# Optimization experiments

Measured on AMD Instinct MI355X. Metric: run time of the kernel, lower is better.

The kernel has to match this reference:

```python
import jax, jax.numpy as jnp
import numpy as np

B, CIN, H, W = 16, 1024, 32, 32
WIDTH = 256          # bottleneck width = planes * base_width/64 * cardinality
OUT = 1024           # planes * expansion
HEADS = WIDTH // 8   # 32
KS = 3               # kernel_size of SelfAttLayer


def unfold3x3(x):
    # x: (B, C, H, W) -> (B, C, 9, H, W), torch.nn.Unfold(3, padding=1) ordering (row-major kernel)
    xp = jnp.pad(x, ((0, 0), (0, 0), (1, 1), (1, 1)))
    h, w = x.shape[2], x.shape[3]
    patches = [xp[:, :, i:i + h, j:j + w] for i in range(KS) for j in range(KS)]
    return jnp.stack(patches, axis=2)


def bn(x, s, b):
    # inference-mode BatchNorm2d with running stats folded into per-channel scale/bias
    return x * s[None, :, None, None] + b[None, :, None, None]


def conv1x1(x, w):
    # w: (Cout, Cin)
    return jnp.einsum('bchw,oc->bohw', x, w)


def setup_inputs() -> dict:
    key = jax.random.key(0)
    ks = jax.random.split(key, 16)
    f = lambda k, shp, scale: (jax.random.normal(k, shp, dtype=jnp.float32) * scale)
    inp = {
        'x': f(ks[0], (B, CIN, H, W), 1.0),
        'w_conv1': f(ks[1], (WIDTH, CIN), 1.0 / np.sqrt(CIN)),
        'bn1_s': jnp.ones((WIDTH,), jnp.float32), 'bn1_b': jnp.zeros((WIDTH,), jnp.float32),
        'wq': f(ks[2], (WIDTH, WIDTH), 1.0 / np.sqrt(WIDTH)),
        'bnq_s': jnp.ones((WIDTH,), jnp.float32), 'bnq_b': jnp.zeros((WIDTH,), jnp.float32),
        'wk': f(ks[3], (WIDTH, WIDTH), 1.0 / np.sqrt(WIDTH)),
        'bnk_s': jnp.ones((WIDTH,), jnp.float32), 'bnk_b': jnp.zeros((WIDTH,), jnp.float32),
        'wv': f(ks[4], (WIDTH, WIDTH), 1.0 / np.sqrt(WIDTH)),
        'bnv_s': jnp.ones((WIDTH,), jnp.float32), 'bnv_b': jnp.zeros((WIDTH,), jnp.float32),
        'pos_h': f(ks[5], (WIDTH, KS, 1), 1.0),
        'pos_w': f(ks[6], (WIDTH, 1, KS), 1.0),
        'bnatt_s': jnp.ones((WIDTH,), jnp.float32), 'bnatt_b': jnp.zeros((WIDTH,), jnp.float32),
        'w_conv3': f(ks[7], (OUT, WIDTH), 1.0 / np.sqrt(WIDTH)),
        'bn3_s': jnp.ones((OUT,), jnp.float32), 'bn3_b': jnp.zeros((OUT,), jnp.float32),
    }
    return inp


def self_att(x, wq, bnq_s, bnq_b, wk, bnk_s, bnk_b, wv, bnv_s, bnv_b,
             pos_h, pos_w, bnatt_s, bnatt_b):
    b, c, h, w = x.shape
    d = c // HEADS
    q = jax.nn.relu(bn(conv1x1(x, wq), bnq_s, bnq_b))          # (B,C,H,W)
    k = jax.nn.relu(bn(conv1x1(x, wk), bnk_s, bnk_b))          # key_ks=1 -> 1x1 conv
    v = bn(conv1x1(x, wv), bnv_s, bnv_b)
    unfold_k = unfold3x3(k)                                     # (B,C,9,H,W)
    pos = (pos_h + pos_w).reshape(1, c, KS * KS, 1, 1)          # (1,C,9,1,1)
    kp = (unfold_k + pos).reshape(b, HEADS, d, KS * KS, h, w)
    qh = q.reshape(b, HEADS, d, h, w)
    attn = jnp.einsum('bgdhw,bgdkhw->bgkhw', qh, kp)            # (B,heads,9,H,W)
    attn = jax.nn.softmax(attn, axis=2)
    # local conv: each channel-group of size d shares its head's attention weights
    v_unf = unfold3x3(v).reshape(b, HEADS, d, KS * KS, h, w)
    out = jnp.einsum('bgdkhw,bgkhw->bgdhw', v_unf, attn).reshape(b, c, h, w)
    return jax.nn.relu(bn(out, bnatt_s, bnatt_b))


def reference(x, w_conv1, bn1_s, bn1_b, wq, bnq_s, bnq_b, wk, bnk_s, bnk_b,
              wv, bnv_s, bnv_b, pos_h, pos_w, bnatt_s, bnatt_b,
              w_conv3, bn3_s, bn3_b):
    residual = x
    h = jax.nn.relu(bn(conv1x1(x, w_conv1), bn1_s, bn1_b))
    h = self_att(h, wq, bnq_s, bnq_b, wk, bnk_s, bnk_b, wv, bnv_s, bnv_b,
                 pos_h, pos_w, bnatt_s, bnatt_b)
    h = bn(conv1x1(h, w_conv3), bn3_s, bn3_b)
    return jax.nn.relu(h + residual)
```

## Files before the change

kernel.cpp:

```cpp
#include <hip/hip_runtime.h>
#include <stdint.h>


typedef __attribute__((ext_vector_type(4))) float f32x4;
typedef __attribute__((ext_vector_type(8))) __bf16 bf16x8;
typedef __attribute__((ext_vector_type(4))) unsigned short u16x4;
typedef __attribute__((ext_vector_type(8))) unsigned short u16x8;

__device__ __forceinline__ float bf2f(unsigned short u) {
  union { unsigned int i; float f; } c; c.i = ((unsigned int)u) << 16; return c.f;
}
__device__ __forceinline__ unsigned short f2bf(float f) {
  union { float f; unsigned int i; } c; c.f = f;
  unsigned int x = c.i;
  return (unsigned short)((x + 0x7FFFu + ((x >> 16) & 1u)) >> 16);
}

__global__ __launch_bounds__(256) void k_transpose_x(const float* __restrict__ x,
                                                     unsigned short* __restrict__ xt) {
  __shared__ float tile[32][33];
  const int b  = blockIdx.z;
  const int c0 = blockIdx.y * 32;
  const int p0 = blockIdx.x * 32;
  const int tx = threadIdx.x & 31;
  const int ty = threadIdx.x >> 5;
  const float* xb = x + (size_t)b * 1048576;
  unsigned short* xtb = xt + (size_t)b * 1048576;
#pragma unroll
  for (int i = 0; i < 4; ++i)
    tile[ty + i * 8][tx] = xb[(size_t)(c0 + ty + i * 8) * 1024 + p0 + tx];
  __syncthreads();
#pragma unroll
  for (int i = 0; i < 4; ++i)
    xtb[(size_t)(p0 + ty + i * 8) * 1024 + c0 + tx] = f2bf(tile[tx][ty + i * 8]);
}

template <int MODE>
__global__ __launch_bounds__(256, 4) void k_gemm(
    const float* __restrict__ A, const unsigned short* __restrict__ B,
    void* __restrict__ CoutV, const float* __restrict__ scale,
    const float* __restrict__ bias, const float* __restrict__ resid,
    int K, int do_relu) {
  __shared__ unsigned short lA[2][64 * 32];
  __shared__ unsigned short lB[2][64 * 32];
  const int m0  = blockIdx.y * 64;
  const int n0  = blockIdx.x * 64;
  const int tid = threadIdx.x;
  const int lane = tid & 63;
  const int wid  = tid >> 6;
  const int wm = (wid >> 1) * 32, wn = (wid & 1) * 32;
  const int fr = lane & 15, fq = lane >> 4;

  f32x4 acc[2][2] = {};

  const int r = tid >> 2;
  const int g = tid & 3;
  const float*          Ag = A + (size_t)(m0 + r) * K + g * 8;
  const unsigned short* Bg = B + (size_t)(n0 + r) * K + g * 8;
  const int lofs = r * 32 + (g ^ (r & 3)) * 8;

  f32x4 a4[2];
  u16x8 bv;
  a4[0] = *(const f32x4*)(Ag);
  a4[1] = *(const f32x4*)(Ag + 4);
  bv    = *(const u16x8*)(Bg);

  int p = 0;
  for (int k0 = 0; k0 < K; k0 += 32, p ^= 1) {
    u16x8 ap;
#pragma unroll
    for (int i = 0; i < 8; ++i) ap[i] = f2bf(a4[i >> 2][i & 3]);
    *(u16x8*)&lA[p][lofs] = ap;
    *(u16x8*)&lB[p][lofs] = bv;
    if (k0 + 32 < K) {
      a4[0] = *(const f32x4*)(Ag + k0 + 32);
      a4[1] = *(const f32x4*)(Ag + k0 + 36);
      bv    = *(const u16x8*)(Bg + k0 + 32);
    }
    __syncthreads();

    bf16x8 af[2], bb[2];
#pragma unroll
    for (int i = 0; i < 2; ++i) {
      const int row = wm + i * 16 + fr;
      af[i] = *(const bf16x8*)&lA[p][row * 32 + (fq ^ (row & 3)) * 8];
    }
#pragma unroll
    for (int j = 0; j < 2; ++j) {
      const int row = wn + j * 16 + fr;
      bb[j] = *(const bf16x8*)&lB[p][row * 32 + (fq ^ (row & 3)) * 8];
    }
#pragma unroll
    for (int i = 0; i < 2; ++i)
#pragma unroll
      for (int j = 0; j < 2; ++j)
        acc[i][j] = __builtin_amdgcn_mfma_f32_16x16x32_bf16(af[i], bb[j], acc[i][j], 0, 0, 0);
  }

#pragma unroll
  for (int i = 0; i < 2; ++i) {
    const int ob = m0 + wm + i * 16 + fq * 4;
    const f32x4 s4 = *(const f32x4*)&scale[ob];
    const f32x4 b4 = *(const f32x4*)&bias[ob];
#pragma unroll
    for (int j = 0; j < 2; ++j) {
      const int P = n0 + wn + j * 16 + fr;
      if (MODE == 0) {
        unsigned short* Cout = (unsigned short*)CoutV;
        u16x4 pk;
#pragma unroll
        for (int rr = 0; rr < 4; ++rr) {
          float v = acc[i][j][rr] * s4[rr] + b4[rr];
          if (do_relu) v = fmaxf(v, 0.0f);
          pk[rr] = f2bf(v);
        }
        *(u16x4*)&Cout[(size_t)P * 256 + ob] = pk;
      } else {
        float* Cout = (float*)CoutV;
        const size_t base = (size_t)(P >> 10) * 1048576 + (size_t)(P & 1023);
#pragma unroll
        for (int rr = 0; rr < 4; ++rr) {
          const size_t addr = base + (size_t)(ob + rr) * 1024;
          float v = acc[i][j][rr] * s4[rr] + b4[rr] + resid[addr];
          Cout[addr] = fmaxf(v, 0.0f);
        }
      }
    }
  }
}

__global__ __launch_bounds__(256, 4) void k_attn(
    const unsigned short* __restrict__ Q, const unsigned short* __restrict__ Kb,
    const unsigned short* __restrict__ Vb, unsigned short* __restrict__ O,
    const float* __restrict__ pos_h, const float* __restrict__ pos_w,
    const float* __restrict__ bs, const float* __restrict__ bb) {
  __shared__ float ph_l[3][256];
  __shared__ float pw_l[3][256];
  {
    const int c = threadIdx.x;
#pragma unroll
    for (int i = 0; i < 3; ++i) {
      ph_l[i][c] = pos_h[c * 3 + i];
      pw_l[i][c] = pos_w[c * 3 + i];
    }
  }
  __syncthreads();
  const int tid = threadIdx.x;
  const int g = tid & 31, s = tid >> 5;
  const int P = blockIdx.x * 8 + s;
  const int b = P >> 10, pix = P & 1023;
  const int hh = pix >> 5, ww = pix & 31;
  const int c0 = g * 8;

  float qf[8];
  {
    u16x8 qv = *(const u16x8*)&Q[(size_t)P * 256 + c0];
#pragma unroll
    for (int d = 0; d < 8; ++d) qf[d] = bf2f(qv[d]);
  }
  float Ai[3], Bj[3];
#pragma unroll
  for (int i = 0; i < 3; ++i) {
    float a = 0.f, w = 0.f;
#pragma unroll
    for (int d = 0; d < 8; ++d) {
      a += qf[d] * ph_l[i][c0 + d];
      w += qf[d] * pw_l[i][c0 + d];
    }
    Ai[i] = a; Bj[i] = w;
  }

  float S[9];
  int nPs[9];
#pragma unroll
  for (int t = 0; t < 9; ++t) {
    const int di = t / 3, dj = t % 3;
    const int nh = hh + di - 1, nw = ww + dj - 1;
    float sum = Ai[di] + Bj[dj];
    int nP = -1;
    if ((unsigned)nh < 32u && (unsigned)nw < 32u) {
      nP = (b << 10) + (nh << 5) + nw;
      u16x8 kv = *(const u16x8*)&Kb[(size_t)nP * 256 + c0];
#pragma unroll
      for (int d = 0; d < 8; ++d) sum += qf[d] * bf2f(kv[d]);
    }
    nPs[t] = nP;
    S[t] = sum;
  }

  float mx = S[0];
#pragma unroll
  for (int t = 1; t < 9; ++t) mx = fmaxf(mx, S[t]);
  float e[9], tot = 0.f;
#pragma unroll
  for (int t = 0; t < 9; ++t) { e[t] = __expf(S[t] - mx); tot += e[t]; }
  const float inv = 1.0f / tot;

  float of[8] = {0.f, 0.f, 0.f, 0.f, 0.f, 0.f, 0.f, 0.f};
#pragma unroll
  for (int t = 0; t < 9; ++t) {
    if (nPs[t] >= 0) {
      u16x8 vv = *(const u16x8*)&Vb[(size_t)nPs[t] * 256 + c0];
      const float w = e[t] * inv;
#pragma unroll
      for (int d = 0; d < 8; ++d) of[d] += w * bf2f(vv[d]);
    }
  }

  u16x8 res;
#pragma unroll
  for (int d = 0; d < 8; ++d) {
    float v = of[d] * bs[c0 + d] + bb[c0 + d];
    v = fmaxf(v, 0.0f);
    res[d] = f2bf(v);
  }
  *(u16x8*)&O[(size_t)P * 256 + c0] = res;
}

extern "C" void kernel_launch(void* const* d_in, const int* in_sizes, int n_in,
                              void* d_out, int out_size, void* d_ws, size_t ws_size,
                              hipStream_t stream) {
  (void)in_sizes; (void)n_in; (void)out_size; (void)ws_size;
  const float* x       = (const float*)d_in[0];
  const float* w1      = (const float*)d_in[1];
  const float* bn1_s   = (const float*)d_in[2];
  const float* bn1_b   = (const float*)d_in[3];
  const float* wq      = (const float*)d_in[4];
  const float* bnq_s   = (const float*)d_in[5];
  const float* bnq_b   = (const float*)d_in[6];
  const float* wk      = (const float*)d_in[7];
  const float* bnk_s   = (const float*)d_in[8];
  const float* bnk_b   = (const float*)d_in[9];
  const float* wv      = (const float*)d_in[10];
  const float* bnv_s   = (const float*)d_in[11];
  const float* bnv_b   = (const float*)d_in[12];
  const float* pos_h   = (const float*)d_in[13];
  const float* pos_w   = (const float*)d_in[14];
  const float* bnatt_s = (const float*)d_in[15];
  const float* bnatt_b = (const float*)d_in[16];
  const float* w3      = (const float*)d_in[17];
  const float* bn3_s   = (const float*)d_in[18];
  const float* bn3_b   = (const float*)d_in[19];

  char* ws = (char*)d_ws;
  unsigned short* h1t = (unsigned short*)(ws);
  unsigned short* qt  = (unsigned short*)(ws + 8388608);
  unsigned short* ktt = (unsigned short*)(ws + 16777216);
  unsigned short* vtt = (unsigned short*)(ws + 25165824);
  unsigned short* att = h1t;
  unsigned short* xt  = (unsigned short*)d_out;

  k_transpose_x<<<dim3(32, 32, 16), dim3(256), 0, stream>>>(x, xt);

  k_gemm<0><<<dim3(256, 4), dim3(256), 0, stream>>>(w1, xt, h1t, bn1_s, bn1_b,
                                                    nullptr, 1024, 1);
  k_gemm<0><<<dim3(256, 4), dim3(256), 0, stream>>>(wq, h1t, qt, bnq_s, bnq_b,
                                                    nullptr, 256, 1);
  k_gemm<0><<<dim3(256, 4), dim3(256), 0, stream>>>(wk, h1t, ktt, bnk_s, bnk_b,
                                                    nullptr, 256, 1);
  k_gemm<0><<<dim3(256, 4), dim3(256), 0, stream>>>(wv, h1t, vtt, bnv_s, bnv_b,
                                                    nullptr, 256, 0);

  k_attn<<<dim3(2048), dim3(256), 0, stream>>>(qt, ktt, vtt, att, pos_h, pos_w,
                                               bnatt_s, bnatt_b);

  k_gemm<1><<<dim3(256, 16), dim3(256), 0, stream>>>(w3, att, d_out,
                                                     bn3_s, bn3_b, x, 256, 1);
}
```

Before: 118.1 us.

## Fuse Q/K/V projections into one launch with a resident K=256 weight tile

Merges the three separate Q, K and V 1x1-conv GEMMs into a single launch that picks its weight, scale and bias by segment of blockIdx.y. It adds a K=256 GEMM variant that converts a full 64x256 weight tile to bf16 into LDS once per block and reuses it across four 64-column N tiles, streaming only the activation operand. The same kernel is used for conv3 with the residual epilogue. The goals are fewer launches, less repeated weight loading and conversion, and fewer blocks. The cost is a larger LDS footprint, which may lower occupancy, and fewer blocks in the grid.

```diff
diff --git a/kernel.cpp b/kernel.cpp
--- a/kernel.cpp
+++ b/kernel.cpp
@@ -35,12 +35,10 @@
     xtb[(size_t)(p0 + ty + i * 8) * 1024 + c0 + tx] = f2bf(tile[tx][ty + i * 8]);
 }
 
-template <int MODE>
-__global__ __launch_bounds__(256, 4) void k_gemm(
+__global__ __launch_bounds__(256, 4) void k_gemm_stream(
     const float* __restrict__ A, const unsigned short* __restrict__ B,
-    void* __restrict__ CoutV, const float* __restrict__ scale,
-    const float* __restrict__ bias, const float* __restrict__ resid,
-    int K, int do_relu) {
+    unsigned short* __restrict__ Cout, const float* __restrict__ scale,
+    const float* __restrict__ bias, int K) {
   __shared__ unsigned short lA[2][64 * 32];
   __shared__ unsigned short lB[2][64 * 32];
   const int m0  = blockIdx.y * 64;
@@ -105,24 +103,131 @@
 #pragma unroll
     for (int j = 0; j < 2; ++j) {
       const int P = n0 + wn + j * 16 + fr;
-      if (MODE == 0) {
-        unsigned short* Cout = (unsigned short*)CoutV;
-        u16x4 pk;
-#pragma unroll
-        for (int rr = 0; rr < 4; ++rr) {
-          float v = acc[i][j][rr] * s4[rr] + b4[rr];
-          if (do_relu) v = fmaxf(v, 0.0f);
-          pk[rr] = f2bf(v);
-        }
-        *(u16x4*)&Cout[(size_t)P * 256 + ob] = pk;
-      } else {
-        float* Cout = (float*)CoutV;
-        const size_t base = (size_t)(P >> 10) * 1048576 + (size_t)(P & 1023);
-#pragma unroll
-        for (int rr = 0; rr < 4; ++rr) {
-          const size_t addr = base + (size_t)(ob + rr) * 1024;
-          float v = acc[i][j][rr] * s4[rr] + b4[rr] + resid[addr];
-          Cout[addr] = fmaxf(v, 0.0f);
+      u16x4 pk;
+#pragma unroll
+      for (int rr = 0; rr < 4; ++rr) {
+        float v = fmaxf(acc[i][j][rr] * s4[rr] + b4[rr], 0.0f);
+        pk[rr] = f2bf(v);
+      }
+      *(u16x4*)&Cout[(size_t)P * 256 + ob] = pk;
+    }
+  }
+}
+
+template <int MODE, int NT>
+__global__ __launch_bounds__(256, 4) void k_gemm_k256(
+    const float* __restrict__ A0, const float* __restrict__ A1,
+    const float* __restrict__ A2, const unsigned short* __restrict__ B,
+    void* __restrict__ CoutV,
+    const float* __restrict__ s0, const float* __restrict__ s1,
+    const float* __restrict__ s2, const float* __restrict__ b0,
+    const float* __restrict__ b1, const float* __restrict__ b2,
+    const float* __restrict__ resid) {
+  __shared__ unsigned short lA[64 * 256];
+  __shared__ unsigned short lB[2][64 * 32];
+  const int mt = blockIdx.y;
+  int seg, m_loc, do_relu;
+  const float *A, *sc, *bi;
+  if (MODE == 0) {
+    seg = mt >> 2; m_loc = (mt & 3) * 64;
+    A  = seg == 0 ? A0 : (seg == 1 ? A1 : A2);
+    sc = seg == 0 ? s0 : (seg == 1 ? s1 : s2);
+    bi = seg == 0 ? b0 : (seg == 1 ? b1 : b2);
+    do_relu = (seg < 2);
+  } else {
+    seg = 0; m_loc = mt * 64; A = A0; sc = s0; bi = b0; do_relu = 1;
+  }
+  const int tid = threadIdx.x;
+  const int lane = tid & 63, wid = tid >> 6;
+  const int wm = (wid >> 1) * 32, wn = (wid & 1) * 32;
+  const int fr = lane & 15, fq = lane >> 4;
+
+  {
+    const int rA = tid >> 2, qd = tid & 3;
+    const float* Ag = A + (size_t)(m_loc + rA) * 256 + qd * 64;
+#pragma unroll
+    for (int m = 0; m < 8; ++m) {
+      f32x4 lo = *(const f32x4*)(Ag + m * 8);
+      f32x4 hi = *(const f32x4*)(Ag + m * 8 + 4);
+      u16x8 pk;
+#pragma unroll
+      for (int e = 0; e < 4; ++e) pk[e] = f2bf(lo[e]);
+#pragma unroll
+      for (int e = 0; e < 4; ++e) pk[4 + e] = f2bf(hi[e]);
+      const int cg = qd * 8 + m;
+      *(u16x8*)&lA[rA * 256 + (cg ^ ((rA & 7) << 2)) * 8] = pk;
+    }
+  }
+
+  const int rB = tid >> 2, gB = tid & 3;
+  const int lofsB = rB * 32 + (gB ^ (rB & 3)) * 8;
+  const int n0_blk = blockIdx.x * NT * 64;
+  const unsigned short* Bg = B + (size_t)(n0_blk + rB) * 256 + gB * 8;
+
+  u16x8 bv = *(const u16x8*)(Bg);
+  f32x4 acc[2][2] = {};
+  int p = 0;
+  const int TOT = NT * 8;
+
+  for (int s = 0; s < TOT; ++s) {
+    const int k0 = (s & 7) * 32;
+    *(u16x8*)&lB[p][lofsB] = bv;
+    if (s + 1 < TOT) {
+      const int s1i = s + 1;
+      bv = *(const u16x8*)(Bg + (size_t)(s1i >> 3) * 16384 + (s1i & 7) * 32);
+    }
+    __syncthreads();
+
+    bf16x8 af[2], bb[2];
+#pragma unroll
+    for (int i = 0; i < 2; ++i) {
+      const int row = wm + i * 16 + fr;
+      const int cg = (k0 >> 3) + fq;
+      af[i] = *(const bf16x8*)&lA[row * 256 + (cg ^ ((row & 7) << 2)) * 8];
+    }
+#pragma unroll
+    for (int j = 0; j < 2; ++j) {
+      const int row = wn + j * 16 + fr;
+      bb[j] = *(const bf16x8*)&lB[p][row * 32 + (fq ^ (row & 3)) * 8];
+    }
+#pragma unroll
+    for (int i = 0; i < 2; ++i)
+#pragma unroll
+      for (int j = 0; j < 2; ++j)
+        acc[i][j] = __builtin_amdgcn_mfma_f32_16x16x32_bf16(af[i], bb[j], acc[i][j], 0, 0, 0);
+    p ^= 1;
+
+    if ((s & 7) == 7) {
+      const int n0 = n0_blk + (s >> 3) * 64;
+#pragma unroll
+      for (int i = 0; i < 2; ++i) {
+        const int ol = m_loc + wm + i * 16 + fq * 4;
+        const f32x4 s4 = *(const f32x4*)&sc[ol];
+        const f32x4 b4 = *(const f32x4*)&bi[ol];
+#pragma unroll
+        for (int j = 0; j < 2; ++j) {
+          const int P = n0 + wn + j * 16 + fr;
+          if (MODE == 0) {
+            unsigned short* Cout = (unsigned short*)CoutV + (size_t)seg * 4194304;
+            u16x4 pk;
+#pragma unroll
+            for (int rr = 0; rr < 4; ++rr) {
+              float v = acc[i][j][rr] * s4[rr] + b4[rr];
+              if (do_relu) v = fmaxf(v, 0.0f);
+              pk[rr] = f2bf(v);
+            }
+            *(u16x4*)&Cout[(size_t)P * 256 + ol] = pk;
+          } else {
+            float* Cout = (float*)CoutV;
+            const size_t base = (size_t)(P >> 10) * 1048576 + (size_t)(P & 1023);
+#pragma unroll
+            for (int rr = 0; rr < 4; ++rr) {
+              const size_t addr = base + (size_t)(ol + rr) * 1024;
+              float v = acc[i][j][rr] * s4[rr] + b4[rr] + resid[addr];
+              Cout[addr] = fmaxf(v, 0.0f);
+            }
+          }
+          acc[i][j] = (f32x4){0.f, 0.f, 0.f, 0.f};
         }
       }
     }
@@ -245,25 +350,20 @@
   char* ws = (char*)d_ws;
   unsigned short* h1t = (unsigned short*)(ws);
   unsigned short* qt  = (unsigned short*)(ws + 8388608);
-  unsigned short* ktt = (unsigned short*)(ws + 16777216);
-  unsigned short* vtt = (unsigned short*)(ws + 25165824);
   unsigned short* att = h1t;
   unsigned short* xt  = (unsigned short*)d_out;
 
   k_transpose_x<<<dim3(32, 32, 16), dim3(256), 0, stream>>>(x, xt);
 
-  k_gemm<0><<<dim3(256, 4), dim3(256), 0, stream>>>(w1, xt, h1t, bn1_s, bn1_b,
-                                                    nullptr, 1024, 1);
-  k_gemm<0><<<dim3(256, 4), dim3(256), 0, stream>>>(wq, h1t, qt, bnq_s, bnq_b,
-                                                    nullptr, 256, 1);
-  k_gemm<0><<<dim3(256, 4), dim3(256), 0, stream>>>(wk, h1t, ktt, bnk_s, bnk_b,
-                                                    nullptr, 256, 1);
-  k_gemm<0><<<dim3(256, 4), dim3(256), 0, stream>>>(wv, h1t, vtt, bnv_s, bnv_b,
-                                                    nullptr, 256, 0);
-
-  k_attn<<<dim3(2048), dim3(256), 0, stream>>>(qt, ktt, vtt, att, pos_h, pos_w,
-                                               bnatt_s, bnatt_b);
-
-  k_gemm<1><<<dim3(256, 16), dim3(256), 0, stream>>>(w3, att, d_out,
-                                                     bn3_s, bn3_b, x, 256, 1);
-}
+  k_gemm_stream<<<dim3(256, 4), dim3(256), 0, stream>>>(w1, xt, h1t, bn1_s, bn1_b, 1024);
+
+  k_gemm_k256<0, 4><<<dim3(64, 12), dim3(256), 0, stream>>>(
+      wq, wk, wv, h1t, qt, bnq_s, bnk_s, bnv_s, bnq_b, bnk_b, bnv_b, nullptr);
+
+  k_attn<<<dim3(2048), dim3(256), 0, stream>>>(qt, qt + 4194304, qt + 8388608, att,
+                                               pos_h, pos_w, bnatt_s, bnatt_b);
+
+  k_gemm_k256<1, 4><<<dim3(64, 16), dim3(256), 0, stream>>>(
+      w3, nullptr, nullptr, att, d_out, bn3_s, nullptr, nullptr, bn3_b, nullptr,
+      nullptr, x);
+}
```

Result: faster. 113.3 us (-4.1%).

## Pre-convert weights to bf16, fuse QKV GEMMs, use direct global-to-LDS loads

Applied to the files above, without the earlier changes.

Adds a kernel that converts all weights to bf16 and packs the q/k/v weights, scales and biases into one buffer, so the three QKV projections run as a single GEMM launch with a per-output relu mask. The GEMM now loads its bf16 tiles with global_load_lds straight into a single LDS buffer, replacing the register-staged double buffer, and the MODE 1 kernel prefetches residuals before the K loop. This cuts launches and per-block f32-to-bf16 conversion. In exchange it adds a weight-conversion kernel on every call, an extra barrier per k step, and the swizzled LDS layout is dropped, which may bring bank conflicts.

```diff
diff --git a/kernel.cpp b/kernel.cpp
--- a/kernel.cpp
+++ b/kernel.cpp
@@ -14,6 +14,37 @@
   union { float f; unsigned int i; } c; c.f = f;
   unsigned int x = c.i;
   return (unsigned short)((x + 0x7FFFu + ((x >> 16) & 1u)) >> 16);
+}
+__device__ __forceinline__ void gload_lds16(const unsigned short* g, unsigned short* l) {
+  __builtin_amdgcn_global_load_lds(
+      (const __attribute__((address_space(1))) unsigned int*)(const void*)g,
+      (__attribute__((address_space(3))) unsigned int*)(void*)l, 16, 0, 0);
+}
+
+__global__ void k_convert(const float* __restrict__ w1, const float* __restrict__ wq,
+                          const float* __restrict__ wk, const float* __restrict__ wv,
+                          const float* __restrict__ w3,
+                          const float* __restrict__ sq, const float* __restrict__ sk,
+                          const float* __restrict__ sv, const float* __restrict__ bq,
+                          const float* __restrict__ bk, const float* __restrict__ bv,
+                          unsigned short* __restrict__ w1b, unsigned short* __restrict__ wqkvb,
+                          unsigned short* __restrict__ w3b, float* __restrict__ sqkv,
+                          float* __restrict__ bqkv) {
+  const int idx = blockIdx.x * 256 + threadIdx.x;
+  if (idx < 262144) { w1b[idx] = f2bf(w1[idx]); return; }
+  if (idx < 327680) { wqkvb[idx - 262144] = f2bf(wq[idx - 262144]); return; }
+  if (idx < 393216) { wqkvb[idx - 262144] = f2bf(wk[idx - 327680]); return; }
+  if (idx < 458752) { wqkvb[idx - 262144] = f2bf(wv[idx - 393216]); return; }
+  if (idx < 720896) { w3b[idx - 458752] = f2bf(w3[idx - 458752]); return; }
+  if (idx < 721664) {
+    const int i = idx - 720896;
+    sqkv[i] = i < 256 ? sq[i] : (i < 512 ? sk[i - 256] : sv[i - 512]);
+    return;
+  }
+  if (idx < 722432) {
+    const int i = idx - 721664;
+    bqkv[i] = i < 256 ? bq[i] : (i < 512 ? bk[i - 256] : bv[i - 512]);
+  }
 }
 
 __global__ __launch_bounds__(256) void k_transpose_x(const float* __restrict__ x,
@@ -36,77 +67,75 @@
 }
 
 template <int MODE>
-__global__ __launch_bounds__(256, 4) void k_gemm(
-    const float* __restrict__ A, const unsigned short* __restrict__ B,
+__global__ __launch_bounds__(256, 4) void k_gemm64(
+    const unsigned short* __restrict__ A, const unsigned short* __restrict__ B,
     void* __restrict__ CoutV, const float* __restrict__ scale,
     const float* __restrict__ bias, const float* __restrict__ resid,
-    int K, int do_relu) {
-  __shared__ unsigned short lA[2][64 * 32];
-  __shared__ unsigned short lB[2][64 * 32];
-  const int m0  = blockIdx.y * 64;
-  const int n0  = blockIdx.x * 64;
+    int K, int relu_mask) {
+  __shared__ unsigned short lA[64 * 32];
+  __shared__ unsigned short lB[64 * 32];
+  const int m0 = blockIdx.y * 64;
+  const int n0 = blockIdx.x * 64;
   const int tid = threadIdx.x;
-  const int lane = tid & 63;
-  const int wid  = tid >> 6;
+  const int lane = tid & 63, wid = tid >> 6;
   const int wm = (wid >> 1) * 32, wn = (wid & 1) * 32;
   const int fr = lane & 15, fq = lane >> 4;
 
   f32x4 acc[2][2] = {};
 
-  const int r = tid >> 2;
-  const int g = tid & 3;
-  const float*          Ag = A + (size_t)(m0 + r) * K + g * 8;
-  const unsigned short* Bg = B + (size_t)(n0 + r) * K + g * 8;
-  const int lofs = r * 32 + (g ^ (r & 3)) * 8;
-
-  f32x4 a4[2];
-  u16x8 bv;
-  a4[0] = *(const f32x4*)(Ag);
-  a4[1] = *(const f32x4*)(Ag + 4);
-  bv    = *(const u16x8*)(Bg);
-
-  int p = 0;
-  for (int k0 = 0; k0 < K; k0 += 32, p ^= 1) {
-    u16x8 ap;
-#pragma unroll
-    for (int i = 0; i < 8; ++i) ap[i] = f2bf(a4[i >> 2][i & 3]);
-    *(u16x8*)&lA[p][lofs] = ap;
-    *(u16x8*)&lB[p][lofs] = bv;
-    if (k0 + 32 < K) {
-      a4[0] = *(const f32x4*)(Ag + k0 + 32);
-      a4[1] = *(const f32x4*)(Ag + k0 + 36);
-      bv    = *(const u16x8*)(Bg + k0 + 32);
-    }
+  const unsigned short* Asrc = A + (size_t)(m0 + wid * 16 + (lane >> 2)) * K + (lane & 3) * 8;
+  const unsigned short* Bsrc = B + (size_t)(n0 + wid * 16 + (lane >> 2)) * K + (lane & 3) * 8;
+  unsigned short* lAw = &lA[wid * 512];
+  unsigned short* lBw = &lB[wid * 512];
+
+  float rres[2][2][4];
+  if (MODE == 1) {
+#pragma unroll
+    for (int i = 0; i < 2; ++i) {
+      const int og = m0 + wm + i * 16 + fq * 4;
+#pragma unroll
+      for (int j = 0; j < 2; ++j) {
+        const int P = n0 + wn + j * 16 + fr;
+        const size_t base = (size_t)(P >> 10) * 1048576 + (size_t)(P & 1023);
+#pragma unroll
+        for (int rr = 0; rr < 4; ++rr)
+          rres[i][j][rr] = resid[base + (size_t)(og + rr) * 1024];
+      }
+    }
+  }
+
+  for (int k0 = 0; k0 < K; k0 += 32) {
+    gload_lds16(Asrc + k0, lAw);
+    gload_lds16(Bsrc + k0, lBw);
     __syncthreads();
 
     bf16x8 af[2], bb[2];
 #pragma unroll
-    for (int i = 0; i < 2; ++i) {
-      const int row = wm + i * 16 + fr;
-      af[i] = *(const bf16x8*)&lA[p][row * 32 + (fq ^ (row & 3)) * 8];
-    }
-#pragma unroll
-    for (int j = 0; j < 2; ++j) {
-      const int row = wn + j * 16 + fr;
-      bb[j] = *(const bf16x8*)&lB[p][row * 32 + (fq ^ (row & 3)) * 8];
-    }
+    for (int i = 0; i < 2; ++i)
+      af[i] = *(const bf16x8*)&lA[(wm + i * 16 + fr) * 32 + fq * 8];
+#pragma unroll
+    for (int j = 0; j < 2; ++j)
+      bb[j] = *(const bf16x8*)&lB[(wn + j * 16 + fr) * 32 + fq * 8];
 #pragma unroll
     for (int i = 0; i < 2; ++i)
 #pragma unroll
       for (int j = 0; j < 2; ++j)
         acc[i][j] = __builtin_amdgcn_mfma_f32_16x16x32_bf16(af[i], bb[j], acc[i][j], 0, 0, 0);
+    __syncthreads();
   }
 
 #pragma unroll
   for (int i = 0; i < 2; ++i) {
-    const int ob = m0 + wm + i * 16 + fq * 4;
-    const f32x4 s4 = *(const f32x4*)&scale[ob];
-    const f32x4 b4 = *(const f32x4*)&bias[ob];
+    const int og = m0 + wm + i * 16 + fq * 4;
+    const f32x4 s4 = *(const f32x4*)&scale[og];
+    const f32x4 b4 = *(const f32x4*)&bias[og];
 #pragma unroll
     for (int j = 0; j < 2; ++j) {
       const int P = n0 + wn + j * 16 + fr;
       if (MODE == 0) {
         unsigned short* Cout = (unsigned short*)CoutV;
+        const int do_relu = (relu_mask >> (og >> 8)) & 1;
+        const size_t obase = (size_t)(og >> 8) * 4194304 + (size_t)P * 256 + (og & 255);
         u16x4 pk;
 #pragma unroll
         for (int rr = 0; rr < 4; ++rr) {
@@ -114,15 +143,14 @@
           if (do_relu) v = fmaxf(v, 0.0f);
           pk[rr] = f2bf(v);
         }
-        *(u16x4*)&Cout[(size_t)P * 256 + ob] = pk;
+        *(u16x4*)&Cout[obase] = pk;
       } else {
         float* Cout = (float*)CoutV;
         const size_t base = (size_t)(P >> 10) * 1048576 + (size_t)(P & 1023);
 #pragma unroll
         for (int rr = 0; rr < 4; ++rr) {
-          const size_t addr = base + (size_t)(ob + rr) * 1024;
-          float v = acc[i][j][rr] * s4[rr] + b4[rr] + resid[addr];
-          Cout[addr] = fmaxf(v, 0.0f);
+          float v = acc[i][j][rr] * s4[rr] + b4[rr] + rres[i][j][rr];
+          Cout[base + (size_t)(og + rr) * 1024] = fmaxf(v, 0.0f);
         }
       }
     }
@@ -243,27 +271,31 @@
   const float* bn3_b   = (const float*)d_in[19];
 
   char* ws = (char*)d_ws;
-  unsigned short* h1t = (unsigned short*)(ws);
-  unsigned short* qt  = (unsigned short*)(ws + 8388608);
-  unsigned short* ktt = (unsigned short*)(ws + 16777216);
-  unsigned short* vtt = (unsigned short*)(ws + 25165824);
-  unsigned short* att = h1t;
-  unsigned short* xt  = (unsigned short*)d_out;
+  unsigned short* h1t   = (unsigned short*)(ws);
+  unsigned short* qkvt  = (unsigned short*)(ws + 8388608);
+  unsigned short* att   = (unsigned short*)(ws + 33554432);
+  unsigned short* xt    = (unsigned short*)(ws + 41943040);
+  unsigned short* w1b   = (unsigned short*)(ws + 75497472);
+  unsigned short* wqkvb = (unsigned short*)(ws + 76021760);
+  unsigned short* w3b   = (unsigned short*)(ws + 76414976);
+  float*          sqkv  = (float*)(ws + 76939264);
+  float*          bqkv  = (float*)(ws + 76942336);
+
+  k_convert<<<dim3(2822), dim3(256), 0, stream>>>(
+      w1, wq, wk, wv, w3, bnq_s, bnk_s, bnv_s, bnq_b, bnk_b, bnv_b,
+      w1b, wqkvb, w3b, sqkv, bqkv);
 
   k_transpose_x<<<dim3(32, 32, 16), dim3(256), 0, stream>>>(x, xt);
 
-  k_gemm<0><<<dim3(256, 4), dim3(256), 0, stream>>>(w1, xt, h1t, bn1_s, bn1_b,
-                                                    nullptr, 1024, 1);
-  k_gemm<0><<<dim3(256, 4), dim3(256), 0, stream>>>(wq, h1t, qt, bnq_s, bnq_b,
-                                                    nullptr, 256, 1);
-  k_gemm<0><<<dim3(256, 4), dim3(256), 0, stream>>>(wk, h1t, ktt, bnk_s, bnk_b,
-                                                    nullptr, 256, 1);
-  k_gemm<0><<<dim3(256, 4), dim3(256), 0, stream>>>(wv, h1t, vtt, bnv_s, bnv_b,
-                                                    nullptr, 256, 0);
-
-  k_attn<<<dim3(2048), dim3(256), 0, stream>>>(qt, ktt, vtt, att, pos_h, pos_w,
-                                               bnatt_s, bnatt_b);
-
-  k_gemm<1><<<dim3(256, 16), dim3(256), 0, stream>>>(w3, att, d_out,
-                                                     bn3_s, bn3_b, x, 256, 1);
-}
+  k_gemm64<0><<<dim3(256, 4), dim3(256), 0, stream>>>(
+      w1b, xt, h1t, bn1_s, bn1_b, nullptr, 1024, 1);
+
+  k_gemm64<0><<<dim3(256, 12), dim3(256), 0, stream>>>(
+      wqkvb, h1t, qkvt, sqkv, bqkv, nullptr, 256, 3);
+
+  k_attn<<<dim3(2048), dim3(256), 0, stream>>>(
+      qkvt, qkvt + 4194304, qkvt + 8388608, att, pos_h, pos_w, bnatt_s, bnatt_b);
+
+  k_gemm64<1><<<dim3(256, 16), dim3(256), 0, stream>>>(
+      w3b, att, d_out, bn3_s, bn3_b, x, 256, 0);
+}
```

Measured after the change: 112.4 us. -4.8%, faster.
